# Performance work log

Measured on AMD Instinct MI355X. Metric: run time of the kernel, lower is better.

## Reference

```python
import jax, jax.numpy as jnp
import numpy as np

N = 100000      # nodes
E = 1600000     # edges (before self-loops)
IN_DIM = 32
HID = 64        # per-head channels of conv1
H1 = 2          # heads of conv1
OUT = 64        # conv2 out channels, heads=1
LN_EPS = 1e-5
NEG_SLOPE = 0.2   # PyG GATConv default LeakyReLU slope


def setup_inputs() -> dict:
    key = jax.random.key(0)
    ks = jax.random.split(key, 13)
    g = lambda k, shape, sc=0.1: (jax.random.normal(k, shape, jnp.float32) * sc)
    return {
        "x": jax.random.normal(ks[0], (N, IN_DIM), jnp.float32),
        "edge_index": jax.random.randint(ks[1], (2, E), 0, N, dtype=jnp.int32),
        # conv1: heads=2, out=HID -> lin weight [IN_DIM, H1*HID], att [H1, HID]
        "W1": g(ks[2], (IN_DIM, H1 * HID)),
        "att_src1": g(ks[3], (H1, HID)),
        "att_dst1": g(ks[4], (H1, HID)),
        "bias1": jnp.zeros((H1 * HID,), jnp.float32),
        # LayerNorm over 128 features
        "gamma": jnp.ones((H1 * HID,), jnp.float32),
        "beta": jnp.zeros((H1 * HID,), jnp.float32),
        # conv2: heads=1, in=128, out=OUT
        "W2": g(ks[5], (H1 * HID, OUT)),
        "att_src2": g(ks[6], (1, OUT)),
        "att_dst2": g(ks[7], (1, OUT)),
        "bias2": jnp.zeros((OUT,), jnp.float32),
    }


def gat_layer(x, src, dst, W, att_src, att_dst, bias, heads, out_ch, n):
    """PyG GATConv (shared src/dst lin, add_self_loops handled by caller)."""
    h = (x @ W).reshape(n, heads, out_ch)                 # [N,H,C]
    a_s = jnp.einsum('nhc,hc->nh', h, att_src)            # [N,H]
    a_d = jnp.einsum('nhc,hc->nh', h, att_dst)
    e = jax.nn.leaky_relu(a_s[src] + a_d[dst], NEG_SLOPE) # [E,H]
    # segment softmax over incoming edges of each destination node
    emax = jax.ops.segment_max(e, dst, num_segments=n)    # [N,H]
    e = jnp.exp(e - emax[dst])
    esum = jax.ops.segment_sum(e, dst, num_segments=n)
    alpha = e / (esum[dst] + 1e-16)                       # [E,H]
    msg = h[src] * alpha[:, :, None]                      # [E,H,C]
    out = jax.ops.segment_sum(msg, dst, num_segments=n)   # [N,H,C]
    return out.reshape(n, heads * out_ch) + bias


def reference(x, edge_index, W1, att_src1, att_dst1, bias1, gamma, beta,
              W2, att_src2, att_dst2, bias2):
    n = x.shape[0]
    loops = jnp.arange(n, dtype=edge_index.dtype)
    src = jnp.concatenate([edge_index[0], loops])         # add self-loops
    dst = jnp.concatenate([edge_index[1], loops])

    h = gat_layer(x, src, dst, W1, att_src1, att_dst1, bias1, H1, HID, n)
    # LayerNorm over feature dim, then ReLU
    mu = h.mean(-1, keepdims=True)
    var = ((h - mu) ** 2).mean(-1, keepdims=True)
    h = (h - mu) * jax.lax.rsqrt(var + LN_EPS) * gamma + beta
    h = jax.nn.relu(h)

    return gat_layer(h, src, dst, W2, att_src2, att_dst2, bias2, 1, OUT, n)
```

## Files before the change

### kernel.cpp

```cpp
#include <hip/hip_runtime.h>
#include <hip/hip_bf16.h>
#include <hip/hip_fp16.h>

#define IN_DIM 32
#define HID 64
#define H1 2
#define F1 (H1 * HID)
#define OUT_CH 64
#define NEG_SLOPE 0.2f
#define LN_EPS 1e-5f

#define BSHIFT 9
#define BMASK ((1 << BSHIFT) - 1)
#define CHUNK 4096
#define CAP 10240

typedef __attribute__((ext_vector_type(8))) short short8x;
typedef __attribute__((ext_vector_type(4))) float floatx4;
typedef __attribute__((ext_vector_type(2))) float floatx2;

__device__ __forceinline__ float leaky(float x) {
    return x > 0.f ? x : NEG_SLOPE * x;
}
__device__ __forceinline__ float bf2f(__hip_bfloat16 v) { return __bfloat162float(v); }
__device__ __forceinline__ short f2bs(float v) {
    __hip_bfloat16 t = __float2bfloat16(v);
    return *reinterpret_cast<short*>(&t);
}
__device__ __forceinline__ void pk_fma(floatx2& c, floatx2 a, floatx2 b) {
    asm("v_pk_fma_f32 %0, %1, %2, %0" : "+v"(c) : "v"(a), "v"(b));
}

__global__ __launch_bounds__(256) void k_bucket_pack(const int* __restrict__ src,
                                                     const int* __restrict__ dst,
                                                     int E, int nb, int nchunk,
                                                     int* __restrict__ bfill,
                                                     unsigned int* __restrict__ bedge,
                                                     const float* __restrict__ W1,
                                                     const float* __restrict__ W2,
                                                     const float* __restrict__ att_s,
                                                     const float* __restrict__ att_d,
                                                     __hip_bfloat16* __restrict__ W1t,
                                                     __hip_bfloat16* __restrict__ W2t,
                                                     float* __restrict__ wsd) {
    int t = threadIdx.x;
    if ((int)blockIdx.x >= nchunk) {
        int idx = ((int)blockIdx.x - nchunk) * 256 + t;
        if (idx < IN_DIM * F1) {
            int ch = idx >> 5, k = idx & 31;
            W1t[idx] = __float2bfloat16(W1[k * F1 + ch]);
        }
        if (idx < F1 * OUT_CH) {
            int ch = idx >> 7, k = idx & 127;
            W2t[idx] = __float2bfloat16(W2[k * OUT_CH + ch]);
        }
        if (idx < 128) {
            int v = idx >> 5;
            int k = idx & 31;
            const float* att = (v & 2) ? att_d : att_s;
            int h = v & 1;
            float s = 0.f;
#pragma unroll 8
            for (int c = 0; c < HID; c++)
                s = fmaf(W1[k * F1 + h * HID + c], att[h * HID + c], s);
            wsd[v * 32 + k] = s;
        }
        return;
    }
    __shared__ int h[512];
    __shared__ int gb[512];
    for (int i = t; i < nb; i += 256) h[i] = 0;
    __syncthreads();
    int base = blockIdx.x * CHUNK;
    unsigned int pk[16];
    int rk[16], bk[16];
#pragma unroll
    for (int j = 0; j < 16; j++) {
        int e = base + j * 256 + t;
        if (e < E) {
            int d = dst[e];
            int b = d >> BSHIFT;
            bk[j] = b;
            pk[j] = ((unsigned)src[e] << BSHIFT) | (unsigned)(d & BMASK);
            rk[j] = atomicAdd(&h[b], 1);
        } else bk[j] = -1;
    }
    __syncthreads();
    for (int i = t; i < nb; i += 256)
        gb[i] = h[i] ? atomicAdd(&bfill[i], h[i]) : 0;
    __syncthreads();
#pragma unroll
    for (int j = 0; j < 16; j++)
        if (bk[j] >= 0) {
            int pos = gb[bk[j]] + rk[j];
            if (pos < CAP) bedge[(size_t)bk[j] * CAP + pos] = pk[j];
        }
}

__global__ __launch_bounds__(256) void k_csr_att1(const unsigned int* __restrict__ bedge,
                                                  const int* __restrict__ bfill, int n, int nb,
                                                  int* __restrict__ cnt,
                                                  int* __restrict__ rowptr,
                                                  int* __restrict__ col,
                                                  const float* __restrict__ x,
                                                  const float* __restrict__ wsd,
                                                  __hip_bfloat16* __restrict__ xb16,
                                                  float2* __restrict__ as1,
                                                  float2* __restrict__ ad1) {
    int t = threadIdx.x;
    if ((int)blockIdx.x >= nb) {
        int node = ((int)blockIdx.x - nb) * 256 + t;
        if (node >= n) return;
        const float4* xp = (const float4*)(x + (size_t)node * IN_DIM);
        float4 xr[8];
#pragma unroll
        for (int i = 0; i < 8; i++) xr[i] = xp[i];
        const float* xf = (const float*)xr;
        short8x* xo = (short8x*)(xb16 + (size_t)node * IN_DIM);
#pragma unroll
        for (int i = 0; i < 4; i++) {
            short8x xb;
#pragma unroll
            for (int j = 0; j < 8; j++) xb[j] = f2bs(xf[i * 8 + j]);
            xo[i] = xb;
        }
        float d0 = 0.f, d1 = 0.f, d2 = 0.f, d3 = 0.f;
#pragma unroll
        for (int k = 0; k < 32; k++) {
            float xv = xf[k];
            d0 = fmaf(xv, wsd[k], d0);
            d1 = fmaf(xv, wsd[32 + k], d1);
            d2 = fmaf(xv, wsd[64 + k], d2);
            d3 = fmaf(xv, wsd[96 + k], d3);
        }
        as1[node] = make_float2(d0, d1);
        ad1[node] = make_float2(d2, d3);
        return;
    }
    int b = blockIdx.x;
    __shared__ int lcnt[512];
    __shared__ int lscan[256];
    int nbase = b << BSHIFT;
    lcnt[2 * t] = 0; lcnt[2 * t + 1] = 0;
    __syncthreads();
    int estart = b * CAP;
    int eend = estart + min(bfill[b], CAP);
    for (int e = estart + t; e < eend; e += 256)
        atomicAdd(&lcnt[bedge[e] & BMASK], 1);
    __syncthreads();
    int c0 = lcnt[2 * t], c1 = lcnt[2 * t + 1];
    int s = c0 + c1;
    lscan[t] = s;
    __syncthreads();
    for (int off = 1; off < 256; off <<= 1) {
        int u = (t >= off) ? lscan[t - off] : 0;
        __syncthreads();
        lscan[t] += u;
        __syncthreads();
    }
    int ex = lscan[t] - s;
    int node0 = nbase + 2 * t, node1 = node0 + 1;
    if (node0 < n) { cnt[node0] = c0; rowptr[node0] = estart + ex; }
    if (node1 < n) { cnt[node1] = c1; rowptr[node1] = estart + ex + c0; }
    __syncthreads();
    lcnt[2 * t] = ex;
    lcnt[2 * t + 1] = ex + c0;
    __syncthreads();
    for (int e = estart + t; e < eend; e += 256) {
        unsigned int p = bedge[e];
        int pos = estart + atomicAdd(&lcnt[p & BMASK], 1);
        col[pos] = (int)(p >> BSHIFT);
    }
}

__global__ __launch_bounds__(256) void k_agg1x(const __hip_bfloat16* __restrict__ xb16,
                                               const float2* __restrict__ as1p,
                                               const float2* __restrict__ ad1p,
                                               const int* __restrict__ rowptr,
                                               const int* __restrict__ cnt,
                                               const int* __restrict__ col,
                                               __hip_bfloat16* __restrict__ a, int n) {
    int wave = threadIdx.x >> 6;
    int lane = threadIdx.x & 63;
    int g = lane >> 4;
    int gl = lane & 15;
    int node = blockIdx.x * 16 + wave * 4 + g;
    bool valid = node < n;
    int nc = valid ? node : 0;
    float2 adn = ad1p[nc];
    float2 asn = as1p[nc];
    const __hip_bfloat162* xv2 = (const __hip_bfloat162*)xb16;
    float w0 = __expf(leaky(asn.x + adn.x));
    float w1 = __expf(leaky(asn.y + adn.y));
    __hip_bfloat162 hv = xv2[(size_t)nc * 16 + gl];
    float x0 = bf2f(hv.x), x1 = bf2f(hv.y);
    float a00 = w0 * x0, a01 = w0 * x1;
    float a10 = w1 * x0, a11 = w1 * x1;
    float ws0 = w0, ws1 = w1;
    int start = valid ? rowptr[nc] : 0;
    int deg = valid ? cnt[nc] : 0;
    int mx = deg;
    mx = max(mx, __shfl_xor(mx, 16, 64));
    mx = max(mx, __shfl_xor(mx, 32, 64));
    int gbase = g << 4;
    for (int base = 0; base < mx; base += 16) {
        int m = deg - base;
        int colv = 0; unsigned wvv = 0u;
        if (gl < m) {
            colv = col[start + base + gl];
            float2 as = as1p[colv];
            float e0 = __expf(leaky(as.x + adn.x));
            float e1 = __expf(leaky(as.y + adn.y));
            wvv = ((unsigned)__half_as_ushort(__float2half(e1)) << 16)
                | (unsigned)__half_as_ushort(__float2half(e0));
        }
        int kend = min(16, mx - base);
        int k = 0;
        for (; k + 8 <= kend; k += 8) {
            int sx[8]; unsigned uw[8];
#pragma unroll
            for (int q = 0; q < 8; q++) {
                sx[q] = __shfl(colv, gbase + k + q);
                uw[q] = __shfl(wvv, gbase + k + q);
            }
            __hip_bfloat162 gx[8];
#pragma unroll
            for (int q = 0; q < 8; q++) gx[q] = xv2[(size_t)sx[q] * 16 + gl];
#pragma unroll
            for (int q = 0; q < 8; q++) {
                float ww0 = __half2float(__ushort_as_half((unsigned short)(uw[q] & 0xffffu)));
                float ww1 = __half2float(__ushort_as_half((unsigned short)(uw[q] >> 16)));
                float gx0 = bf2f(gx[q].x), gx1 = bf2f(gx[q].y);
                a00 = fmaf(ww0, gx0, a00); a01 = fmaf(ww0, gx1, a01);
                a10 = fmaf(ww1, gx0, a10); a11 = fmaf(ww1, gx1, a11);
                ws0 += ww0; ws1 += ww1;
            }
        }
        for (; k < kend; k++) {
            int s = __shfl(colv, gbase + k);
            unsigned u = __shfl(wvv, gbase + k);
            __hip_bfloat162 gxx = xv2[(size_t)s * 16 + gl];
            float ww0 = __half2float(__ushort_as_half((unsigned short)(u & 0xffffu)));
            float ww1 = __half2float(__ushort_as_half((unsigned short)(u >> 16)));
            float gx0 = bf2f(gxx.x), gx1 = bf2f(gxx.y);
            a00 = fmaf(ww0, gx0, a00); a01 = fmaf(ww0, gx1, a01);
            a10 = fmaf(ww1, gx0, a10); a11 = fmaf(ww1, gx1, a11);
            ws0 += ww0; ws1 += ww1;
        }
    }
    if (valid) {
        float inv0 = 1.f / (ws0 + 1e-16f);
        float inv1 = 1.f / (ws1 + 1e-16f);
        __hip_bfloat162* ao = (__hip_bfloat162*)(a + (size_t)node * 64);
        __hip_bfloat162 o0, o1;
        o0.x = __float2bfloat16(a00 * inv0); o0.y = __float2bfloat16(a01 * inv0);
        o1.x = __float2bfloat16(a10 * inv1); o1.y = __float2bfloat16(a11 * inv1);
        ao[gl] = o0;
        ao[16 + gl] = o1;
    }
}

__global__ __launch_bounds__(256) void k_ln1node2(const __hip_bfloat16* __restrict__ a,
                                                  const __hip_bfloat16* __restrict__ W1t,
                                                  const float* __restrict__ bias1,
                                                  const float* __restrict__ gamma,
                                                  const float* __restrict__ beta,
                                                  const __hip_bfloat16* __restrict__ W2t,
                                                  const float* __restrict__ att_s2,
                                                  const float* __restrict__ att_d2,
                                                  __hip_bfloat16* __restrict__ h2b,
                                                  float* __restrict__ as2,
                                                  float* __restrict__ ad2, int n) {
    __shared__ __hip_bfloat16 hs[64][136];
    int wave = threadIdx.x >> 6;
    int lane = threadIdx.x & 63;
    int row16 = lane & 15;
    int quad = lane >> 4;
    int node0 = blockIdx.x * 64 + wave * 16;

    {
        short8x bfr[8];
#pragma unroll
        for (int nt = 0; nt < 8; nt++)
            bfr[nt] = *(const short8x*)(W1t + (nt * 16 + row16) * IN_DIM + quad * 8);

        int arow = node0 + row16;
        if (arow >= n) arow = n - 1;
        const __hip_bfloat16* ap = a + (size_t)arow * 64 + quad * 8;
        short8x af0 = *(const short8x*)ap;
        short8x af1 = *(const short8x*)(ap + 32);

        floatx4 acc[8];
#pragma unroll
        for (int nt = 0; nt < 8; nt++) acc[nt] = (floatx4){0.f, 0.f, 0.f, 0.f};
#pragma unroll
        for (int nt = 0; nt < 8; nt++)
            acc[nt] = __builtin_amdgcn_mfma_f32_16x16x32_bf16(nt < 4 ? af0 : af1, bfr[nt],
                                                              acc[nt], 0, 0, 0);

        float bv[8], gv[8], btv[8];
#pragma unroll
        for (int nt = 0; nt < 8; nt++) {
            int ch = nt * 16 + row16;
            bv[nt] = bias1[ch];
            gv[nt] = gamma[ch];
            btv[nt] = beta[ch];
        }
#pragma unroll
        for (int rr = 0; rr < 4; rr++) {
            int node = node0 + quad * 4 + rr;
            float v[8];
            float sum = 0.f, sq = 0.f;
#pragma unroll
            for (int nt = 0; nt < 8; nt++) {
                v[nt] = acc[nt][rr] + bv[nt];
                sum += v[nt];
                sq += v[nt] * v[nt];
            }
#pragma unroll
            for (int off = 1; off < 16; off <<= 1) {
                sum += __shfl_xor(sum, off, 64);
                sq += __shfl_xor(sq, off, 64);
            }
            float mu = sum * (1.f / 128.f);
            float var = sq * (1.f / 128.f) - mu * mu;
            float r = rsqrtf(var + LN_EPS);
            if (node < n) {
                int lr = wave * 16 + quad * 4 + rr;
#pragma unroll
                for (int nt = 0; nt < 8; nt++) {
                    float o = (v[nt] - mu) * r * gv[nt] + btv[nt];
                    hs[lr][nt * 16 + row16] = __float2bfloat16(fmaxf(o, 0.f));
                }
            }
        }
    }
    __syncthreads();

    short8x bfr2[4][4];
#pragma unroll
    for (int nt = 0; nt < 4; nt++) {
        const __hip_bfloat16* wrow = W2t + (nt * 16 + row16) * F1 + quad * 8;
#pragma unroll
        for (int kc = 0; kc < 4; kc++)
            bfr2[kc][nt] = *(const short8x*)(wrow + kc * 32);
    }

    floatx4 acc2[4];
#pragma unroll
    for (int nt = 0; nt < 4; nt++) acc2[nt] = (floatx4){0.f, 0.f, 0.f, 0.f};

    int lrow = wave * 16 + row16;
#pragma unroll
    for (int kc = 0; kc < 4; kc++) {
        short8x af = *(const short8x*)&hs[lrow][quad * 8 + kc * 32];
#pragma unroll
        for (int nt = 0; nt < 4; nt++)
            acc2[nt] = __builtin_amdgcn_mfma_f32_16x16x32_bf16(af, bfr2[kc][nt], acc2[nt],
                                                               0, 0, 0);
    }

    float asv[4], adv[4];
#pragma unroll
    for (int nt = 0; nt < 4; nt++) {
        asv[nt] = att_s2[nt * 16 + row16];
        adv[nt] = att_d2[nt * 16 + row16];
    }
#pragma unroll
    for (int rr = 0; rr < 4; rr++) {
        int node = node0 + quad * 4 + rr;
        float ps = 0.f, pd = 0.f;
#pragma unroll
        for (int nt = 0; nt < 4; nt++) {
            float v = acc2[nt][rr];
            if (node < n) h2b[(size_t)node * OUT_CH + nt * 16 + row16] = __float2bfloat16(v);
            ps = fmaf(v, asv[nt], ps);
            pd = fmaf(v, adv[nt], pd);
        }
#pragma unroll
        for (int off = 1; off < 16; off <<= 1) {
            ps += __shfl_xor(ps, off, 64);
            pd += __shfl_xor(pd, off, 64);
        }
        if (row16 == 0 && node < n) { as2[node] = ps; ad2[node] = pd; }
    }
}

__global__ __launch_bounds__(256) void k_agg2(const __hip_bfloat16* __restrict__ h2b,
                                              const float* __restrict__ as2,
                                              const float* __restrict__ ad2,
                                              const int* __restrict__ rowptr,
                                              const int* __restrict__ cnt,
                                              const int* __restrict__ col,
                                              const float* __restrict__ bias2,
                                              float* __restrict__ out, int n) {
    int node = blockIdx.x * 4 + (threadIdx.x >> 6);
    int lane = threadIdx.x & 63;
    if (node >= n) return;
    int c = lane & 15;
    int quarter = lane >> 4;
    const unsigned* h2u = (const unsigned*)h2b;
    float adn = ad2[node];
    float wself = __expf(leaky(as2[node] + adn));
    floatx2 accA = {0.f, 0.f}, accB = {0.f, 0.f};
    if (quarter == 0) {
        uint2 su = *(const uint2*)(h2u + (size_t)node * 32 + c * 2);
        accA.x = wself * __uint_as_float(su.x << 16);
        accA.y = wself * __uint_as_float(su.x & 0xffff0000u);
        accB.x = wself * __uint_as_float(su.y << 16);
        accB.y = wself * __uint_as_float(su.y & 0xffff0000u);
    }
    float wsum = wself;
    int start = rowptr[node], deg = cnt[node];
    for (int base = 0; base < deg; base += 64) {
        int m = min(64, deg - base);
        int colv = 0; float wvv = 0.f;
        if (lane < m) {
            colv = col[start + base + lane];
            wvv = __expf(leaky(as2[colv] + adn));
        }
        float r = wvv;
#pragma unroll
        for (int off = 1; off < 64; off <<= 1) r += __shfl_xor(r, off, 64);
        wsum += r;
        int P = (m + 3) >> 2;
        int p = 0;
        for (; p + 4 <= P; p += 4) {
            int sx[4]; float wx[4];
#pragma unroll
            for (int u = 0; u < 4; u++) {
                int idx = 4 * (p + u) + quarter;
                sx[u] = __shfl(colv, idx);
                wx[u] = __shfl(wvv, idx);
            }
            uint2 gu[4];
#pragma unroll
            for (int u = 0; u < 4; u++)
                gu[u] = *(const uint2*)(h2u + (size_t)sx[u] * 32 + c * 2);
#pragma unroll
            for (int u = 0; u < 4; u++) {
                floatx2 wp = {wx[u], wx[u]};
                floatx2 g0 = {__uint_as_float(gu[u].x << 16),
                              __uint_as_float(gu[u].x & 0xffff0000u)};
                floatx2 g1 = {__uint_as_float(gu[u].y << 16),
                              __uint_as_float(gu[u].y & 0xffff0000u)};
                pk_fma(accA, wp, g0);
                pk_fma(accB, wp, g1);
            }
        }
        for (; p < P; p++) {
            int idx = 4 * p + quarter;
            int s = __shfl(colv, idx);
            float wk = __shfl(wvv, idx);
            uint2 u2 = *(const uint2*)(h2u + (size_t)s * 32 + c * 2);
            floatx2 wp = {wk, wk};
            floatx2 g0 = {__uint_as_float(u2.x << 16),
                          __uint_as_float(u2.x & 0xffff0000u)};
            floatx2 g1 = {__uint_as_float(u2.y << 16),
                          __uint_as_float(u2.y & 0xffff0000u)};
            pk_fma(accA, wp, g0);
            pk_fma(accB, wp, g1);
        }
    }
#pragma unroll
    for (int off = 16; off <= 32; off <<= 1) {
        accA.x += __shfl_xor(accA.x, off, 64);
        accA.y += __shfl_xor(accA.y, off, 64);
        accB.x += __shfl_xor(accB.x, off, 64);
        accB.y += __shfl_xor(accB.y, off, 64);
    }
    float inv = 1.f / (wsum + 1e-16f);
    if (quarter == 0) {
        float4 bv = ((const float4*)bias2)[c];
        float4 ov;
        ov.x = accA.x * inv + bv.x;
        ov.y = accA.y * inv + bv.y;
        ov.z = accB.x * inv + bv.z;
        ov.w = accB.y * inv + bv.w;
        ((float4*)out)[(size_t)node * 16 + c] = ov;
    }
}

extern "C" void kernel_launch(void* const* d_in, const int* in_sizes, int n_in,
                              void* d_out, int out_size, void* d_ws, size_t ws_size,
                              hipStream_t stream) {
    const float* x        = (const float*)d_in[0];
    const int*   eidx     = (const int*)d_in[1];
    const float* W1       = (const float*)d_in[2];
    const float* att_src1 = (const float*)d_in[3];
    const float* att_dst1 = (const float*)d_in[4];
    const float* bias1    = (const float*)d_in[5];
    const float* gamma    = (const float*)d_in[6];
    const float* beta     = (const float*)d_in[7];
    const float* W2       = (const float*)d_in[8];
    const float* att_src2 = (const float*)d_in[9];
    const float* att_dst2 = (const float*)d_in[10];
    const float* bias2    = (const float*)d_in[11];
    float* out = (float*)d_out;

    const int N = in_sizes[0] / IN_DIM;
    const int E = in_sizes[1] / 2;
    const int* src = eidx;
    const int* dst = eidx + E;
    const int nb = (N + BMASK) >> BSHIFT;

    char* w = (char*)d_ws;
    __hip_bfloat16* xb16  = (__hip_bfloat16*)w;  w += (size_t)N * IN_DIM * 2;
    __hip_bfloat16* a     = (__hip_bfloat16*)w;  w += (size_t)N * 64 * 2;
    __hip_bfloat16* h2b   = (__hip_bfloat16*)w;  w += (size_t)N * OUT_CH * 2;
    __hip_bfloat16* W1t   = (__hip_bfloat16*)w;  w += IN_DIM * F1 * 2;
    __hip_bfloat16* W2t   = (__hip_bfloat16*)w;  w += F1 * OUT_CH * 2;
    float* wsd = (float*)w; w += 128 * 4;
    float* as1 = (float*)w; w += (size_t)N * 2 * 4;
    float* ad1 = (float*)w; w += (size_t)N * 2 * 4;
    float* as2 = (float*)w; w += (size_t)N * 4;
    float* ad2 = (float*)w; w += (size_t)N * 4;
    int* cnt    = (int*)w; w += (size_t)N * 4;
    int* rowptr = (int*)w; w += (size_t)N * 4;
    int* bfill  = (int*)w; w += 512 * 4;
    int* col    = (int*)w; w += (size_t)nb * CAP * 4;
    unsigned int* bedge = (unsigned int*)w; w += (size_t)nb * CAP * 4;

    const int nchunk = (E + CHUNK - 1) / CHUNK;

    hipMemsetAsync(bfill, 0, 512 * 4, stream);
    k_bucket_pack<<<nchunk + 32, 256, 0, stream>>>(src, dst, E, nb, nchunk, bfill, bedge,
                                                   W1, W2, att_src1, att_dst1,
                                                   W1t, W2t, wsd);
    k_csr_att1<<<nb + (N + 255) / 256, 256, 0, stream>>>(bedge, bfill, N, nb,
                                                         cnt, rowptr, col,
                                                         x, wsd, xb16,
                                                         (float2*)as1, (float2*)ad1);
    k_agg1x<<<(N + 15) / 16, 256, 0, stream>>>(xb16, (const float2*)as1, (const float2*)ad1,
                                               rowptr, cnt, col, a, N);
    k_ln1node2<<<(N + 63) / 64, 256, 0, stream>>>(a, W1t, bias1, gamma, beta,
                                                  W2t, att_src2, att_dst2,
                                                  h2b, as2, ad2, N);
    k_agg2<<<(N + 3) / 4, 256, 0, stream>>>(h2b, as2, ad2,
                                            rowptr, cnt, col, bias2, out, N);
}
```

Baseline: 245.7 us.

## Map four nodes per wave in layer-2 aggregation with 16-lane groups

The layer-2 aggregation kernel now gives each destination node a 16-lane group, so one wave handles four nodes instead of one. Each group loads its own neighbor indices and computes their attention weights, then gathers all edges itself in batches of eight. This drops the cross-quarter reduction of the accumulators at the end. Average degree is about 17, so the old one-node-per-wave layout left most lanes idle during weight computation. In exchange, the loop runs to the largest degree among the four nodes, so groups sharing a wave stall on imbalanced degrees.

```diff
diff --git a/kernel.cpp b/kernel.cpp
--- a/kernel.cpp
+++ b/kernel.cpp
@@ -394,65 +394,68 @@
                                               const int* __restrict__ col,
                                               const float* __restrict__ bias2,
                                               float* __restrict__ out, int n) {
-    int node = blockIdx.x * 4 + (threadIdx.x >> 6);
+    int wave = threadIdx.x >> 6;
     int lane = threadIdx.x & 63;
-    if (node >= n) return;
-    int c = lane & 15;
-    int quarter = lane >> 4;
+    int g = lane >> 4;
+    int gl = lane & 15;
+    int node = blockIdx.x * 16 + wave * 4 + g;
+    bool valid = node < n;
+    int nc = valid ? node : 0;
     const unsigned* h2u = (const unsigned*)h2b;
-    float adn = ad2[node];
-    float wself = __expf(leaky(as2[node] + adn));
-    floatx2 accA = {0.f, 0.f}, accB = {0.f, 0.f};
-    if (quarter == 0) {
-        uint2 su = *(const uint2*)(h2u + (size_t)node * 32 + c * 2);
-        accA.x = wself * __uint_as_float(su.x << 16);
-        accA.y = wself * __uint_as_float(su.x & 0xffff0000u);
-        accB.x = wself * __uint_as_float(su.y << 16);
-        accB.y = wself * __uint_as_float(su.y & 0xffff0000u);
-    }
+    float adn = ad2[nc];
+    float wself = __expf(leaky(as2[nc] + adn));
+    uint2 su = *(const uint2*)(h2u + (size_t)nc * 32 + gl * 2);
+    floatx2 wsp = {wself, wself};
+    floatx2 accA = {wself * __uint_as_float(su.x << 16),
+                    wself * __uint_as_float(su.x & 0xffff0000u)};
+    floatx2 accB = {wself * __uint_as_float(su.y << 16),
+                    wself * __uint_as_float(su.y & 0xffff0000u)};
     float wsum = wself;
-    int start = rowptr[node], deg = cnt[node];
-    for (int base = 0; base < deg; base += 64) {
-        int m = min(64, deg - base);
+    int start = valid ? rowptr[nc] : 0;
+    int deg = valid ? cnt[nc] : 0;
+    int mx = deg;
+    mx = max(mx, __shfl_xor(mx, 16, 64));
+    mx = max(mx, __shfl_xor(mx, 32, 64));
+    int gbase = g << 4;
+    for (int base = 0; base < mx; base += 16) {
+        int m = deg - base;
         int colv = 0; float wvv = 0.f;
-        if (lane < m) {
-            colv = col[start + base + lane];
+        if (gl < m) {
+            colv = col[start + base + gl];
             wvv = __expf(leaky(as2[colv] + adn));
         }
         float r = wvv;
 #pragma unroll
-        for (int off = 1; off < 64; off <<= 1) r += __shfl_xor(r, off, 64);
+        for (int off = 1; off < 16; off <<= 1) r += __shfl_xor(r, off, 64);
         wsum += r;
-        int P = (m + 3) >> 2;
-        int p = 0;
-        for (; p + 4 <= P; p += 4) {
-            int sx[4]; float wx[4];
-#pragma unroll
-            for (int u = 0; u < 4; u++) {
-                int idx = 4 * (p + u) + quarter;
-                sx[u] = __shfl(colv, idx);
-                wx[u] = __shfl(wvv, idx);
-            }
-            uint2 gu[4];
-#pragma unroll
-            for (int u = 0; u < 4; u++)
-                gu[u] = *(const uint2*)(h2u + (size_t)sx[u] * 32 + c * 2);
-#pragma unroll
-            for (int u = 0; u < 4; u++) {
-                floatx2 wp = {wx[u], wx[u]};
-                floatx2 g0 = {__uint_as_float(gu[u].x << 16),
-                              __uint_as_float(gu[u].x & 0xffff0000u)};
-                floatx2 g1 = {__uint_as_float(gu[u].y << 16),
-                              __uint_as_float(gu[u].y & 0xffff0000u)};
+        int kend = min(16, mx - base);
+        int k = 0;
+        for (; k + 8 <= kend; k += 8) {
+            int sx[8]; float wx[8];
+#pragma unroll
+            for (int q = 0; q < 8; q++) {
+                sx[q] = __shfl(colv, gbase + k + q);
+                wx[q] = __shfl(wvv, gbase + k + q);
+            }
+            uint2 gu[8];
+#pragma unroll
+            for (int q = 0; q < 8; q++)
+                gu[q] = *(const uint2*)(h2u + (size_t)sx[q] * 32 + gl * 2);
+#pragma unroll
+            for (int q = 0; q < 8; q++) {
+                floatx2 wp = {wx[q], wx[q]};
+                floatx2 g0 = {__uint_as_float(gu[q].x << 16),
+                              __uint_as_float(gu[q].x & 0xffff0000u)};
+                floatx2 g1 = {__uint_as_float(gu[q].y << 16),
+                              __uint_as_float(gu[q].y & 0xffff0000u)};
                 pk_fma(accA, wp, g0);
                 pk_fma(accB, wp, g1);
             }
         }
-        for (; p < P; p++) {
-            int idx = 4 * p + quarter;
-            int s = __shfl(colv, idx);
-            float wk = __shfl(wvv, idx);
-            uint2 u2 = *(const uint2*)(h2u + (size_t)s * 32 + c * 2);
+        for (; k < kend; k++) {
+            int s = __shfl(colv, gbase + k);
+            float wk = __shfl(wvv, gbase + k);
+            uint2 u2 = *(const uint2*)(h2u + (size_t)s * 32 + gl * 2);
             floatx2 wp = {wk, wk};
             floatx2 g0 = {__uint_as_float(u2.x << 16),
                           __uint_as_float(u2.x & 0xffff0000u)};
@@ -462,22 +465,15 @@
             pk_fma(accB, wp, g1);
         }
     }
-#pragma unroll
-    for (int off = 16; off <= 32; off <<= 1) {
-        accA.x += __shfl_xor(accA.x, off, 64);
-        accA.y += __shfl_xor(accA.y, off, 64);
-        accB.x += __shfl_xor(accB.x, off, 64);
-        accB.y += __shfl_xor(accB.y, off, 64);
-    }
-    float inv = 1.f / (wsum + 1e-16f);
-    if (quarter == 0) {
-        float4 bv = ((const float4*)bias2)[c];
+    if (valid) {
+        float inv = 1.f / (wsum + 1e-16f);
+        float4 bv = ((const float4*)bias2)[gl];
         float4 ov;
         ov.x = accA.x * inv + bv.x;
         ov.y = accA.y * inv + bv.y;
         ov.z = accB.x * inv + bv.z;
         ov.w = accB.y * inv + bv.w;
-        ((float4*)out)[(size_t)node * 16 + c] = ov;
+        ((float4*)out)[(size_t)node * 16 + gl] = ov;
     }
 }
 
@@ -536,6 +532,6 @@
     k_ln1node2<<<(N + 63) / 64, 256, 0, stream>>>(a, W1t, bias1, gamma, beta,
                                                   W2t, att_src2, att_dst2,
                                                   h2b, as2, ad2, N);
-    k_agg2<<<(N + 3) / 4, 256, 0, stream>>>(h2b, as2, ad2,
-                                            rowptr, cnt, col, bias2, out, N);
-}
+    k_agg2<<<(N + 15) / 16, 256, 0, stream>>>(h2b, as2, ad2,
+                                              rowptr, cnt, col, bias2, out, N);
+}
```

After: 226.3 us. 1.09x faster.
